# Performance work log

Measured on AMD Instinct MI355X. Metric: run time of the kernel, lower is better.

Reference implementation:

```python
import math
import jax, jax.numpy as jnp
import numpy as np

N = 100000
E = 800000
IN_DIM = 128
HID = 128
HEADS = 4
C = HID // HEADS  # 32 per-head channels
TD = 16           # time encoding dim
NL = 2            # layers - 1 conv blocks
OUT = 2
BN_EPS = 1e-5


def setup_inputs() -> dict:
    key = jax.random.key(0)
    ks = jax.random.split(key, 24)
    s = 0.05
    inp = {
        "x": jax.random.normal(ks[0], (N, IN_DIM), dtype=jnp.float32),
        "edge_index": jax.random.randint(ks[1], (2, E), 0, N, dtype=jnp.int32),
        "timesteps": jax.random.randint(ks[2], (N,), 0, 100000, dtype=jnp.int32),
        # input projection Linear(in_dim + td, hid)
        "proj_w": jax.random.normal(ks[3], (IN_DIM + TD, HID), dtype=jnp.float32) * s,
        "proj_b": jnp.zeros((HID,), dtype=jnp.float32),
        # GATConv params per layer (stacked over NL layers)
        "conv_w": jax.random.normal(ks[4], (NL, HID, HID), dtype=jnp.float32) * s,
        "conv_b": jnp.zeros((NL, HID), dtype=jnp.float32),
        "att_src": jax.random.normal(ks[5], (NL, HEADS, C), dtype=jnp.float32) * s,
        "att_dst": jax.random.normal(ks[6], (NL, HEADS, C), dtype=jnp.float32) * s,
        # BatchNorm (eval mode: running stats)
        "bn_gamma": jax.random.uniform(ks[7], (NL, HID), dtype=jnp.float32) + 0.5,
        "bn_beta": jax.random.normal(ks[8], (NL, HID), dtype=jnp.float32) * s,
        "bn_mean": jax.random.normal(ks[9], (NL, HID), dtype=jnp.float32) * s,
        "bn_var": jax.random.uniform(ks[10], (NL, HID), dtype=jnp.float32) + 0.5,
        # age gate MLP: Linear(1,16) -> ReLU -> Linear(16,1) -> Sigmoid
        "gate_w1": jax.random.normal(ks[11], (1, 16), dtype=jnp.float32) * 0.5,
        "gate_b1": jnp.zeros((16,), dtype=jnp.float32),
        "gate_w2": jax.random.normal(ks[12], (16, 1), dtype=jnp.float32) * 0.5,
        "gate_b2": jnp.zeros((1,), dtype=jnp.float32),
        # head: Linear(hid, hid//2) -> ReLU -> Linear(hid//2, out)
        "head_w1": jax.random.normal(ks[13], (HID, HID // 2), dtype=jnp.float32) * s,
        "head_b1": jnp.zeros((HID // 2,), dtype=jnp.float32),
        "head_w2": jax.random.normal(ks[14], (HID // 2, OUT), dtype=jnp.float32) * s,
        "head_b2": jnp.zeros((OUT,), dtype=jnp.float32),
    }
    return inp


def _time_enc(t):
    # t: [N] float -> [N, TD] sinusoidal encoding
    t = t[:, None]
    freqs = jnp.exp(jnp.arange(0, TD, 2, dtype=jnp.float32) * (-(math.log(10000.0) / TD)))
    return jnp.concatenate([jnp.sin(t * freqs), jnp.cos(t * freqs)], axis=-1)


def _gat_conv(h_in, src, dst, W, b, a_src, a_dst):
    # h_in: [N, HID]; src/dst: [Etot] with self-loops included
    h = (h_in @ W).reshape(N, HEADS, C)                 # [N, H, C]
    al_s = jnp.sum(h * a_src[None], axis=-1)            # [N, H]
    al_d = jnp.sum(h * a_dst[None], axis=-1)            # [N, H]
    alpha = jax.nn.leaky_relu(al_s[src] + al_d[dst], 0.2)  # [Etot, H]
    # segment softmax over destination nodes
    m = jax.ops.segment_max(alpha, dst, num_segments=N)    # [N, H]
    ex = jnp.exp(alpha - m[dst])
    den = jax.ops.segment_sum(ex, dst, num_segments=N)     # [N, H]
    att = ex / (den[dst] + 1e-16)                          # [Etot, H]
    msg = h[src] * att[:, :, None]                         # [Etot, H, C]
    out = jax.ops.segment_sum(msg, dst, num_segments=N)    # [N, H, C]
    return out.reshape(N, HID) + b


def reference(x, edge_index, timesteps, proj_w, proj_b, conv_w, conv_b,
              att_src, att_dst, bn_gamma, bn_beta, bn_mean, bn_var,
              gate_w1, gate_b1, gate_w2, gate_b2,
              head_w1, head_b1, head_w2, head_b2):
    t = timesteps.astype(jnp.float32)
    te = _time_enc(t)                                      # [N, TD]
    h = jax.nn.relu(jnp.concatenate([x, te], axis=-1) @ proj_w + proj_b)
    # ages in [0, 1]
    mn, mx = jnp.min(t), jnp.max(t)
    ages = ((t - mn) / jnp.maximum(mx - mn, 1.0))[:, None]  # [N, 1]
    gate = jax.nn.sigmoid(jax.nn.relu(ages @ gate_w1 + gate_b1) @ gate_w2 + gate_b2)  # [N, 1]
    # add self-loops (PyG GATConv default)
    loop = jnp.arange(N, dtype=edge_index.dtype)
    src = jnp.concatenate([edge_index[0], loop])
    dst = jnp.concatenate([edge_index[1], loop])
    for i in range(NL):
        h = _gat_conv(h, src, dst, conv_w[i], conv_b[i], att_src[i], att_dst[i])
        h = (h - bn_mean[i]) * (bn_gamma[i] / jnp.sqrt(bn_var[i] + BN_EPS)) + bn_beta[i]
        h = jax.nn.elu(h)
        h = h * gate  # dropout is identity in eval mode
    h = jax.nn.relu(h @ head_w1 + head_b1)
    return h @ head_w2 + head_b2  # [N, OUT]
```

## Files before the change

kernel.cpp:

```cpp
#include <hip/hip_runtime.h>
#include <cfloat>
#include <climits>
#include <cmath>

constexpr int N_ = 100000;
constexpr int E_ = 800000;
constexpr int NBLK_ = (N_ + 255) / 256;

__global__ __launch_bounds__(256) void k_prep(const int* __restrict__ ts, float* __restrict__ te,
                                              int* __restrict__ count, int* __restrict__ bmin,
                                              int* __restrict__ bmax) {
    const float FRQ[8] = {1.0f, 0.31622776601683794f, 0.1f, 0.031622776601683794f,
                          0.01f, 0.0031622776601683794f, 0.001f, 0.00031622776601683794f};
    int n = blockIdx.x * 256 + threadIdx.x;
    int tv_min = INT_MAX, tv_max = INT_MIN;
    if (n < N_) {
        int tv = ts[n];
        tv_min = tv; tv_max = tv;
        count[n] = 1;
        float tf = (float)tv;
#pragma unroll
        for (int j = 0; j < 8; ++j) {
            float sv, cv;
            sincosf(tf * FRQ[j], &sv, &cv);
            te[n * 16 + j] = sv;
            te[n * 16 + 8 + j] = cv;
        }
    }
#pragma unroll
    for (int o = 32; o >= 1; o >>= 1) {
        tv_min = min(tv_min, __shfl_xor(tv_min, o));
        tv_max = max(tv_max, __shfl_xor(tv_max, o));
    }
    __shared__ int smn[4], smx[4];
    if ((threadIdx.x & 63) == 0) {
        smn[threadIdx.x >> 6] = tv_min;
        smx[threadIdx.x >> 6] = tv_max;
    }
    __syncthreads();
    if (threadIdx.x == 0) {
        bmin[blockIdx.x] = min(min(smn[0], smn[1]), min(smn[2], smn[3]));
        bmax[blockIdx.x] = max(max(smx[0], smx[1]), max(smx[2], smx[3]));
    }
}

__global__ __launch_bounds__(256) void k_count(const int* __restrict__ ei, int* __restrict__ count) {
    int e = blockIdx.x * 256 + threadIdx.x;
    if (e < E_) atomicAdd(&count[ei[E_ + e]], 1);
}

__global__ __launch_bounds__(256) void k_bsum(const int* __restrict__ count, int* __restrict__ bsum) {
    int i = blockIdx.x * 256 + threadIdx.x;
    int v = (i < N_) ? count[i] : 0;
#pragma unroll
    for (int o = 32; o >= 1; o >>= 1) v += __shfl_xor(v, o);
    __shared__ int wsum[4];
    if ((threadIdx.x & 63) == 0) wsum[threadIdx.x >> 6] = v;
    __syncthreads();
    if (threadIdx.x == 0) bsum[blockIdx.x] = wsum[0] + wsum[1] + wsum[2] + wsum[3];
}

__global__ __launch_bounds__(512) void k_bscan(int* __restrict__ bsum, int* __restrict__ indptr,
                                               const int* __restrict__ bmin, const int* __restrict__ bmax,
                                               int* __restrict__ minmax) {
    int t = threadIdx.x;
    int v = (t < NBLK_) ? bsum[t] : 0;
    __shared__ int sc[512];
    sc[t] = v;
    __syncthreads();
    for (int o = 1; o < 512; o <<= 1) {
        int u = (t >= o) ? sc[t - o] : 0;
        __syncthreads();
        sc[t] += u;
        __syncthreads();
    }
    if (t < NBLK_) bsum[t] = sc[t] - v;
    if (t == NBLK_ - 1) indptr[N_] = sc[t];
    int mn = (t < NBLK_) ? bmin[t] : INT_MAX;
    int mx = (t < NBLK_) ? bmax[t] : INT_MIN;
#pragma unroll
    for (int o = 32; o >= 1; o >>= 1) {
        mn = min(mn, __shfl_xor(mn, o));
        mx = max(mx, __shfl_xor(mx, o));
    }
    __shared__ int rmn[8], rmx[8];
    if ((t & 63) == 0) { rmn[t >> 6] = mn; rmx[t >> 6] = mx; }
    __syncthreads();
    if (t == 0) {
        int a = INT_MAX, b = INT_MIN;
#pragma unroll
        for (int q = 0; q < 8; ++q) { a = min(a, rmn[q]); b = max(b, rmx[q]); }
        minmax[0] = a;
        minmax[1] = b;
    }
}

__global__ __launch_bounds__(256) void k_scan_c(const int* __restrict__ count, const int* __restrict__ bsum,
                                                int* __restrict__ indptr, int* __restrict__ srcs,
                                                int* __restrict__ cursor, const int* __restrict__ ts,
                                                const int* __restrict__ minmax, const float* __restrict__ gw1,
                                                const float* __restrict__ gb1, const float* __restrict__ gw2,
                                                const float* __restrict__ gb2, float* __restrict__ gate) {
    int t = threadIdx.x;
    int i = blockIdx.x * 256 + t;
    int v = (i < N_) ? count[i] : 0;
    __shared__ int sc[256];
    sc[t] = v;
    __syncthreads();
    for (int o = 1; o < 256; o <<= 1) {
        int u = (t >= o) ? sc[t - o] : 0;
        __syncthreads();
        sc[t] += u;
        __syncthreads();
    }
    if (i < N_) {
        int off = bsum[blockIdx.x] + sc[t] - v;
        indptr[i] = off;
        srcs[off] = i;
        cursor[i] = off + 1;
        float mn = (float)minmax[0], mx = (float)minmax[1];
        float age = ((float)ts[i] - mn) / fmaxf(mx - mn, 1.0f);
        float o2 = gb2[0];
#pragma unroll
        for (int j = 0; j < 16; ++j) {
            float hj = fmaxf(age * gw1[j] + gb1[j], 0.f);
            o2 += hj * gw2[j];
        }
        gate[i] = 1.f / (1.f + __expf(-o2));
    }
}

__global__ __launch_bounds__(256) void k_scatter(const int* __restrict__ ei, int* __restrict__ cursor,
                                                 int* __restrict__ srcs) {
    int e = blockIdx.x * 256 + threadIdx.x;
    if (e < E_) {
        int s = ei[e];
        int d = ei[E_ + e];
        int p = atomicAdd(&cursor[d], 1);
        srcs[p] = s;
    }
}

template <int K, int M, int KC, int MODE>
__global__ __launch_bounds__((M / 4) * 16) void k_gemm(const float* __restrict__ A, const float* __restrict__ te,
                                                       const float* __restrict__ W, const float* __restrict__ bias,
                                                       const float* __restrict__ asrc, const float* __restrict__ adst,
                                                       const float* __restrict__ w2, const float* __restrict__ b2,
                                                       float* __restrict__ Cout, float* __restrict__ al_s,
                                                       float* __restrict__ al_d) {
    constexpr int GR = 128;
    constexpr int CTH = M / 4;
    constexpr int TB = CTH * 16;
    constexpr int NA = (GR * KC / 4) / TB;
    constexpr int NW = (KC * M / 4) / TB;
    constexpr int F4R = KC / 4;
    static_assert(K % KC == 0, "K%KC");
    __shared__ float As[KC][GR + 4];
    __shared__ float Ws[KC][M];
    __shared__ float asl[128], adl[128];
    __shared__ float w2l[128];
    const int r0 = blockIdx.x * GR;
    const int tid = threadIdx.x;
    const int tx = tid % CTH, ty = tid / CTH;
    if (MODE == 1 && tid < 128) { asl[tid] = asrc[tid]; adl[tid] = adst[tid]; }
    if (MODE == 2 && tid < 128) { w2l[tid] = w2[tid]; }
    float acc[8][4];
#pragma unroll
    for (int i = 0; i < 8; ++i)
#pragma unroll
        for (int j = 0; j < 4; ++j) acc[i][j] = 0.f;

    for (int k0 = 0; k0 < K; k0 += KC) {
        float4 pa[NA], pw[NW];
#pragma unroll
        for (int i = 0; i < NA; ++i) {
            int f = tid + i * TB;
            int row = f / F4R, fq = f % F4R;
            int gr = r0 + row;
            float4 v = make_float4(0.f, 0.f, 0.f, 0.f);
            if (gr < N_) {
                if (MODE == 0) {
                    int kg = k0 + fq * 4;
                    if (kg < 128) v = *(const float4*)&A[gr * 128 + kg];
                    else          v = *(const float4*)&te[gr * 16 + (kg - 128)];
                } else {
                    v = *(const float4*)&A[gr * K + k0 + fq * 4];
                }
            }
            pa[i] = v;
        }
#pragma unroll
        for (int i = 0; i < NW; ++i) {
            int f = tid + i * TB;
            int kk = f / (M / 4), c4 = f % (M / 4);
            pw[i] = *(const float4*)&W[(k0 + kk) * M + c4 * 4];
        }
        __syncthreads();
#pragma unroll
        for (int i = 0; i < NA; ++i) {
            int f = tid + i * TB;
            int row = f / F4R, fq = f % F4R;
            As[fq * 4 + 0][row] = pa[i].x;
            As[fq * 4 + 1][row] = pa[i].y;
            As[fq * 4 + 2][row] = pa[i].z;
            As[fq * 4 + 3][row] = pa[i].w;
        }
#pragma unroll
        for (int i = 0; i < NW; ++i) {
            int f = tid + i * TB;
            int kk = f / (M / 4), c4 = f % (M / 4);
            *(float4*)&Ws[kk][c4 * 4] = pw[i];
        }
        __syncthreads();
#pragma unroll
        for (int kk = 0; kk < KC; ++kk) {
            float4 a0 = *(const float4*)&As[kk][ty * 8];
            float4 a1 = *(const float4*)&As[kk][ty * 8 + 4];
            float av[8] = {a0.x, a0.y, a0.z, a0.w, a1.x, a1.y, a1.z, a1.w};
            float4 w = *(const float4*)&Ws[kk][tx * 4];
            float wv[4] = {w.x, w.y, w.z, w.w};
#pragma unroll
            for (int i = 0; i < 8; ++i)
#pragma unroll
                for (int j = 0; j < 4; ++j) acc[i][j] = fmaf(av[i], wv[j], acc[i][j]);
        }
    }

#pragma unroll
    for (int i = 0; i < 8; ++i) {
        int gr = r0 + ty * 8 + i;
        bool valid = gr < N_;
        if (MODE == 0) {
            if (valid) {
                float4 v;
                v.x = fmaxf(acc[i][0] + bias[tx * 4 + 0], 0.f);
                v.y = fmaxf(acc[i][1] + bias[tx * 4 + 1], 0.f);
                v.z = fmaxf(acc[i][2] + bias[tx * 4 + 2], 0.f);
                v.w = fmaxf(acc[i][3] + bias[tx * 4 + 3], 0.f);
                *(float4*)&Cout[gr * M + tx * 4] = v;
            }
        } else if (MODE == 1) {
            if (valid) {
                float4 v = make_float4(acc[i][0], acc[i][1], acc[i][2], acc[i][3]);
                *(float4*)&Cout[gr * M + tx * 4] = v;
            }
            float ps = 0.f, pd = 0.f;
#pragma unroll
            for (int q = 0; q < 4; ++q) {
                int c = tx * 4 + q;
                ps = fmaf(acc[i][q], asl[c], ps);
                pd = fmaf(acc[i][q], adl[c], pd);
            }
#pragma unroll
            for (int o = 1; o <= 4; o <<= 1) {
                ps += __shfl_xor(ps, o);
                pd += __shfl_xor(pd, o);
            }
            if (valid && (tx & 7) == 0) {
                int head = tx >> 3;
                al_s[gr * 4 + head] = ps;
                al_d[gr * 4 + head] = pd;
            }
        } else {
            float ps0 = 0.f, ps1 = 0.f;
#pragma unroll
            for (int q = 0; q < 4; ++q) {
                float hv = fmaxf(acc[i][q] + bias[tx * 4 + q], 0.f);
                int c = tx * 4 + q;
                ps0 = fmaf(hv, w2l[c * 2 + 0], ps0);
                ps1 = fmaf(hv, w2l[c * 2 + 1], ps1);
            }
#pragma unroll
            for (int o = 1; o <= 8; o <<= 1) {
                ps0 += __shfl_xor(ps0, o);
                ps1 += __shfl_xor(ps1, o);
            }
            if (valid && tx == 0) {
                *(float2*)&Cout[gr * 2] = make_float2(ps0 + b2[0], ps1 + b2[1]);
            }
        }
    }
}

__global__ __launch_bounds__(256) void k_gat(const int* __restrict__ indptr, const int* __restrict__ srcs,
                                             const float* __restrict__ al_s, const float* __restrict__ al_d,
                                             const float* __restrict__ h2, const float* __restrict__ convb,
                                             const float* __restrict__ gamma, const float* __restrict__ beta,
                                             const float* __restrict__ mean, const float* __restrict__ var,
                                             const float* __restrict__ gate, float* __restrict__ hout) {
    int g = threadIdx.x >> 4, lg = threadIdx.x & 15;
    int n = blockIdx.x * 16 + g;
    if (n >= N_) return;
    int start = indptr[n], end = indptr[n + 1];
    int hl = lg >> 2;
    int c0 = lg * 8;
    float gn = gate[n];
    float4 ad4 = *(const float4*)&al_d[n * 4];
    float adv[4] = {ad4.x, ad4.y, ad4.z, ad4.w};
    float M[4] = {-FLT_MAX, -FLT_MAX, -FLT_MAX, -FLT_MAX};
    float D[4] = {0.f, 0.f, 0.f, 0.f};
    float ac[8] = {0.f, 0.f, 0.f, 0.f, 0.f, 0.f, 0.f, 0.f};

    for (int p0 = start; p0 < end; p0 += 16) {
        int cs = end - p0;
        if (cs > 16) cs = 16;
        float a[4];
        int s = 0;
        if (lg < cs) {
            s = srcs[p0 + lg];
            float4 as4 = *(const float4*)&al_s[s * 4];
            float asv[4] = {as4.x, as4.y, as4.z, as4.w};
#pragma unroll
            for (int h = 0; h < 4; ++h) {
                float x = asv[h] + adv[h];
                a[h] = x > 0.f ? x : 0.2f * x;
            }
        } else {
#pragma unroll
            for (int h = 0; h < 4; ++h) a[h] = -FLT_MAX;
        }
        float f[4], w[4];
#pragma unroll
        for (int h = 0; h < 4; ++h) {
            float m = a[h];
#pragma unroll
            for (int o = 8; o >= 1; o >>= 1) m = fmaxf(m, __shfl_xor(m, o));
            float Mn = fmaxf(M[h], m);
            f[h] = __expf(M[h] - Mn);
            M[h] = Mn;
            w[h] = __expf(a[h] - Mn);
            float sv = w[h];
#pragma unroll
            for (int o = 8; o >= 1; o >>= 1) sv += __shfl_xor(sv, o);
            D[h] = D[h] * f[h] + sv;
        }
        float fh = hl < 2 ? (hl == 0 ? f[0] : f[1]) : (hl == 2 ? f[2] : f[3]);
        float whl = hl < 2 ? (hl == 0 ? w[0] : w[1]) : (hl == 2 ? w[2] : w[3]);
#pragma unroll
        for (int q = 0; q < 8; ++q) ac[q] *= fh;
        int i = 0;
        for (; i + 1 < cs; i += 2) {
            float w0 = __shfl(whl, i, 16);
            float w1 = __shfl(whl, i + 1, 16);
            int s0 = __shfl(s, i, 16);
            int s1 = __shfl(s, i + 1, 16);
            float4 h0a = *(const float4*)&h2[s0 * 128 + c0];
            float4 h0b = *(const float4*)&h2[s0 * 128 + c0 + 4];
            float4 h1a = *(const float4*)&h2[s1 * 128 + c0];
            float4 h1b = *(const float4*)&h2[s1 * 128 + c0 + 4];
            ac[0] = fmaf(w0, h0a.x, ac[0]); ac[1] = fmaf(w0, h0a.y, ac[1]);
            ac[2] = fmaf(w0, h0a.z, ac[2]); ac[3] = fmaf(w0, h0a.w, ac[3]);
            ac[4] = fmaf(w0, h0b.x, ac[4]); ac[5] = fmaf(w0, h0b.y, ac[5]);
            ac[6] = fmaf(w0, h0b.z, ac[6]); ac[7] = fmaf(w0, h0b.w, ac[7]);
            ac[0] = fmaf(w1, h1a.x, ac[0]); ac[1] = fmaf(w1, h1a.y, ac[1]);
            ac[2] = fmaf(w1, h1a.z, ac[2]); ac[3] = fmaf(w1, h1a.w, ac[3]);
            ac[4] = fmaf(w1, h1b.x, ac[4]); ac[5] = fmaf(w1, h1b.y, ac[5]);
            ac[6] = fmaf(w1, h1b.z, ac[6]); ac[7] = fmaf(w1, h1b.w, ac[7]);
        }
        if (i < cs) {
            float w0 = __shfl(whl, i, 16);
            int s0 = __shfl(s, i, 16);
            float4 h0a = *(const float4*)&h2[s0 * 128 + c0];
            float4 h0b = *(const float4*)&h2[s0 * 128 + c0 + 4];
            ac[0] = fmaf(w0, h0a.x, ac[0]); ac[1] = fmaf(w0, h0a.y, ac[1]);
            ac[2] = fmaf(w0, h0a.z, ac[2]); ac[3] = fmaf(w0, h0a.w, ac[3]);
            ac[4] = fmaf(w0, h0b.x, ac[4]); ac[5] = fmaf(w0, h0b.y, ac[5]);
            ac[6] = fmaf(w0, h0b.z, ac[6]); ac[7] = fmaf(w0, h0b.w, ac[7]);
        }
    }

    float Dh = hl < 2 ? (hl == 0 ? D[0] : D[1]) : (hl == 2 ? D[2] : D[3]);
    float rd = 1.0f / (Dh + 1e-16f);
    float out8[8];
#pragma unroll
    for (int half = 0; half < 2; ++half) {
        int cb0 = c0 + half * 4;
        float4 cb = *(const float4*)&convb[cb0];
        float4 gm = *(const float4*)&gamma[cb0];
        float4 bt = *(const float4*)&beta[cb0];
        float4 mu = *(const float4*)&mean[cb0];
        float4 vr = *(const float4*)&var[cb0];
        float cbv[4] = {cb.x, cb.y, cb.z, cb.w};
        float gmv[4] = {gm.x, gm.y, gm.z, gm.w};
        float btv[4] = {bt.x, bt.y, bt.z, bt.w};
        float muv[4] = {mu.x, mu.y, mu.z, mu.w};
        float vrv[4] = {vr.x, vr.y, vr.z, vr.w};
#pragma unroll
        for (int q = 0; q < 4; ++q) {
            float val = ac[half * 4 + q] * rd + cbv[q];
            float sc = gmv[q] * rsqrtf(vrv[q] + 1e-5f);
            val = (val - muv[q]) * sc + btv[q];
            val = val > 0.f ? val : expm1f(val);
            out8[half * 4 + q] = val * gn;
        }
    }
    *(float4*)&hout[n * 128 + c0] = make_float4(out8[0], out8[1], out8[2], out8[3]);
    *(float4*)&hout[n * 128 + c0 + 4] = make_float4(out8[4], out8[5], out8[6], out8[7]);
}

extern "C" void kernel_launch(void* const* d_in, const int* in_sizes, int n_in,
                              void* d_out, int out_size, void* d_ws, size_t ws_size,
                              hipStream_t stream) {
    const float* x       = (const float*)d_in[0];
    const int*   ei      = (const int*)d_in[1];
    const int*   ts      = (const int*)d_in[2];
    const float* proj_w  = (const float*)d_in[3];
    const float* proj_b  = (const float*)d_in[4];
    const float* conv_w  = (const float*)d_in[5];
    const float* conv_b  = (const float*)d_in[6];
    const float* att_src = (const float*)d_in[7];
    const float* att_dst = (const float*)d_in[8];
    const float* bn_g    = (const float*)d_in[9];
    const float* bn_b    = (const float*)d_in[10];
    const float* bn_m    = (const float*)d_in[11];
    const float* bn_v    = (const float*)d_in[12];
    const float* gw1     = (const float*)d_in[13];
    const float* gb1     = (const float*)d_in[14];
    const float* gw2     = (const float*)d_in[15];
    const float* gb2     = (const float*)d_in[16];
    const float* hw1     = (const float*)d_in[17];
    const float* hb1     = (const float*)d_in[18];
    const float* hw2     = (const float*)d_in[19];
    const float* hb2     = (const float*)d_in[20];
    float* out = (float*)d_out;

    float* ws   = (float*)d_ws;
    float* h    = ws;
    float* h2   = h + (size_t)N_ * 128;
    float* te   = h2 + (size_t)N_ * 128;
    float* al_s = te + (size_t)N_ * 16;
    float* al_d = al_s + (size_t)N_ * 4;
    float* gate = al_d + (size_t)N_ * 4;
    int* indptr = (int*)(gate + N_);
    int* srcs   = indptr + (N_ + 1);
    int* count  = srcs + (N_ + E_);
    int* cursor = count + N_;
    int* bsum   = cursor + N_;
    int* bmin   = bsum + NBLK_;
    int* bmax   = bmin + NBLK_;
    int* minmax = bmax + NBLK_;

    k_prep<<<NBLK_, 256, 0, stream>>>(ts, te, count, bmin, bmax);
    k_count<<<(E_ + 255) / 256, 256, 0, stream>>>(ei, count);
    k_bsum<<<NBLK_, 256, 0, stream>>>(count, bsum);
    k_bscan<<<1, 512, 0, stream>>>(bsum, indptr, bmin, bmax, minmax);
    k_scan_c<<<NBLK_, 256, 0, stream>>>(count, bsum, indptr, srcs, cursor, ts, minmax,
                                        gw1, gb1, gw2, gb2, gate);
    k_scatter<<<(E_ + 255) / 256, 256, 0, stream>>>(ei, cursor, srcs);

    k_gemm<144, 128, 16, 0><<<782, 512, 0, stream>>>(x, te, proj_w, proj_b, nullptr, nullptr,
                                                     nullptr, nullptr, h, nullptr, nullptr);
    for (int l = 0; l < 2; ++l) {
        k_gemm<128, 128, 32, 1><<<782, 512, 0, stream>>>(h, nullptr, conv_w + l * 128 * 128, nullptr,
                                                         att_src + l * 128, att_dst + l * 128,
                                                         nullptr, nullptr, h2, al_s, al_d);
        k_gat<<<(N_ + 15) / 16, 256, 0, stream>>>(indptr, srcs, al_s, al_d, h2, conv_b + l * 128,
                                                  bn_g + l * 128, bn_b + l * 128, bn_m + l * 128,
                                                  bn_v + l * 128, gate, h);
    }
    k_gemm<128, 64, 32, 2><<<782, 256, 0, stream>>>(h, nullptr, hw1, hb1, nullptr, nullptr,
                                                    hw2, hb2, out, nullptr, nullptr);
}
```

Before: 471.5 us.

## Double-buffer GEMM tiles using direct global-to-LDS async loads

Replaces the register-staged, transposed shared-memory tile loads in the fused GEMM kernel with direct global-to-LDS loads via the global_load_lds builtin into double-buffered row-major tiles. The next K-chunk is prefetched while the current one is computed, and one barrier per chunk replaces two. The inner product now reads A rows as float4 along K. The row-major A layout can cause LDS bank conflicts, the out-of-range rows are clamped instead of zeroed, and correctness relies on the builtin's completion semantics at the barrier.

New measurement: 502.6 us. +6.6%, slower.

```diff
diff --git a/kernel.cpp b/kernel.cpp
--- a/kernel.cpp
+++ b/kernel.cpp
@@ -6,6 +6,11 @@
 constexpr int N_ = 100000;
 constexpr int E_ = 800000;
 constexpr int NBLK_ = (N_ + 255) / 256;
+
+#define GLOAD16(gp, lp)                                                        \
+    __builtin_amdgcn_global_load_lds(                                          \
+        (const __attribute__((address_space(1))) void*)(gp),                   \
+        (__attribute__((address_space(3))) void*)(lp), 16, 0, 0)
 
 __global__ __launch_bounds__(256) void k_prep(const int* __restrict__ ts, float* __restrict__ te,
                                               int* __restrict__ count, int* __restrict__ bmin,
@@ -142,6 +147,41 @@
 }
 
 template <int K, int M, int KC, int MODE>
+__device__ __forceinline__ void stage_tile(const float* __restrict__ A, const float* __restrict__ te,
+                                           const float* __restrict__ W, float* as_buf, float* ws_buf,
+                                           int r0, int k0, int wave, int lane) {
+    constexpr int TB = (M / 4) * 16;
+    constexpr int NWAVE = TB / 64;
+    constexpr int ROWB = KC * 4;
+    constexpr int ASEG = (128 * ROWB) / 1024;
+    constexpr int RPS = 1024 / ROWB;
+    constexpr int LPR = ROWB / 16;
+    constexpr int WROWB = M * 4;
+    constexpr int WSEG = (KC * WROWB) / 1024;
+    constexpr int WRPS = 1024 / WROWB;
+    constexpr int WLPR = WROWB / 16;
+    for (int j = wave; j < ASEG; j += NWAVE) {
+        int row = j * RPS + lane / LPR;
+        int gr = r0 + row;
+        if (gr > N_ - 1) gr = N_ - 1;
+        int c4 = lane % LPR;
+        const float* gp;
+        if (MODE == 0) {
+            if (k0 < 128) gp = &A[gr * 128 + k0 + c4 * 4];
+            else          gp = &te[gr * 16 + c4 * 4];
+        } else {
+            gp = &A[gr * K + k0 + c4 * 4];
+        }
+        GLOAD16(gp, as_buf + j * 256);
+    }
+    for (int j = wave; j < WSEG; j += NWAVE) {
+        int kk = j * WRPS + lane / WLPR;
+        int c4 = lane % WLPR;
+        GLOAD16(&W[(k0 + kk) * M + c4 * 4], ws_buf + j * 256);
+    }
+}
+
+template <int K, int M, int KC, int MODE>
 __global__ __launch_bounds__((M / 4) * 16) void k_gemm(const float* __restrict__ A, const float* __restrict__ te,
                                                        const float* __restrict__ W, const float* __restrict__ bias,
                                                        const float* __restrict__ asrc, const float* __restrict__ adst,
@@ -150,18 +190,16 @@
                                                        float* __restrict__ al_d) {
     constexpr int GR = 128;
     constexpr int CTH = M / 4;
-    constexpr int TB = CTH * 16;
-    constexpr int NA = (GR * KC / 4) / TB;
-    constexpr int NW = (KC * M / 4) / TB;
-    constexpr int F4R = KC / 4;
+    constexpr int NCH = K / KC;
     static_assert(K % KC == 0, "K%KC");
-    __shared__ float As[KC][GR + 4];
-    __shared__ float Ws[KC][M];
+    __shared__ __align__(16) float As[2][GR * KC];
+    __shared__ __align__(16) float Ws[2][KC * M];
     __shared__ float asl[128], adl[128];
     __shared__ float w2l[128];
     const int r0 = blockIdx.x * GR;
     const int tid = threadIdx.x;
     const int tx = tid % CTH, ty = tid / CTH;
+    const int wave = tid >> 6, lane = tid & 63;
     if (MODE == 1 && tid < 128) { asl[tid] = asrc[tid]; adl[tid] = adst[tid]; }
     if (MODE == 2 && tid < 128) { w2l[tid] = w2[tid]; }
     float acc[8][4];
@@ -170,60 +208,32 @@
 #pragma unroll
         for (int j = 0; j < 4; ++j) acc[i][j] = 0.f;
 
-    for (int k0 = 0; k0 < K; k0 += KC) {
-        float4 pa[NA], pw[NW];
-#pragma unroll
-        for (int i = 0; i < NA; ++i) {
-            int f = tid + i * TB;
-            int row = f / F4R, fq = f % F4R;
-            int gr = r0 + row;
-            float4 v = make_float4(0.f, 0.f, 0.f, 0.f);
-            if (gr < N_) {
-                if (MODE == 0) {
-                    int kg = k0 + fq * 4;
-                    if (kg < 128) v = *(const float4*)&A[gr * 128 + kg];
-                    else          v = *(const float4*)&te[gr * 16 + (kg - 128)];
-                } else {
-                    v = *(const float4*)&A[gr * K + k0 + fq * 4];
+    stage_tile<K, M, KC, MODE>(A, te, W, As[0], Ws[0], r0, 0, wave, lane);
+    __syncthreads();
+    for (int c = 0; c < NCH; ++c) {
+        const int b = c & 1;
+        if (c + 1 < NCH)
+            stage_tile<K, M, KC, MODE>(A, te, W, As[b ^ 1], Ws[b ^ 1], r0, (c + 1) * KC, wave, lane);
+#pragma unroll
+        for (int q = 0; q < KC / 4; ++q) {
+            float4 ar[8];
+#pragma unroll
+            for (int i = 0; i < 8; ++i)
+                ar[i] = *(const float4*)&As[b][(ty * 8 + i) * KC + q * 4];
+#pragma unroll
+            for (int k2 = 0; k2 < 4; ++k2) {
+                float4 w = *(const float4*)&Ws[b][(q * 4 + k2) * M + tx * 4];
+                float wv[4] = {w.x, w.y, w.z, w.w};
+#pragma unroll
+                for (int i = 0; i < 8; ++i) {
+                    const float* arp = (const float*)&ar[i];
+                    float av = arp[k2];
+#pragma unroll
+                    for (int j = 0; j < 4; ++j) acc[i][j] = fmaf(av, wv[j], acc[i][j]);
                 }
             }
-            pa[i] = v;
-        }
-#pragma unroll
-        for (int i = 0; i < NW; ++i) {
-            int f = tid + i * TB;
-            int kk = f / (M / 4), c4 = f % (M / 4);
-            pw[i] = *(const float4*)&W[(k0 + kk) * M + c4 * 4];
         }
         __syncthreads();
-#pragma unroll
-        for (int i = 0; i < NA; ++i) {
-            int f = tid + i * TB;
-            int row = f / F4R, fq = f % F4R;
-            As[fq * 4 + 0][row] = pa[i].x;
-            As[fq * 4 + 1][row] = pa[i].y;
-            As[fq * 4 + 2][row] = pa[i].z;
-            As[fq * 4 + 3][row] = pa[i].w;
-        }
-#pragma unroll
-        for (int i = 0; i < NW; ++i) {
-            int f = tid + i * TB;
-            int kk = f / (M / 4), c4 = f % (M / 4);
-            *(float4*)&Ws[kk][c4 * 4] = pw[i];
-        }
-        __syncthreads();
-#pragma unroll
-        for (int kk = 0; kk < KC; ++kk) {
-            float4 a0 = *(const float4*)&As[kk][ty * 8];
-            float4 a1 = *(const float4*)&As[kk][ty * 8 + 4];
-            float av[8] = {a0.x, a0.y, a0.z, a0.w, a1.x, a1.y, a1.z, a1.w};
-            float4 w = *(const float4*)&Ws[kk][tx * 4];
-            float wv[4] = {w.x, w.y, w.z, w.w};
-#pragma unroll
-            for (int i = 0; i < 8; ++i)
-#pragma unroll
-                for (int j = 0; j < 4; ++j) acc[i][j] = fmaf(av[i], wv[j], acc[i][j]);
-        }
     }
 
 #pragma unroll
```
